# Performance work log

Hardware: AMD Instinct MI355X
Metric: run time of the kernel (lower is better)

## Reference

```python
import jax, jax.numpy as jnp
import numpy as np

DT = 0.1
WHEELBASE = 2.8
STATE_DIM = 12


def setup_inputs() -> dict:
    key = jax.random.key(0)
    k1, k2, k3 = jax.random.split(key, 3)
    b, l, h = 512, 64, 80
    x0 = jax.random.normal(k1, (b, STATE_DIM), dtype=jnp.float32)
    controls = jax.random.normal(k2, (b, l, h, 3), dtype=jnp.float32)
    deg = jax.random.uniform(k3, (b, 5), dtype=jnp.float32)
    return {"x0": x0, "controls": controls, "deg": deg}


def reference(x0, controls, deg):
    b, l, h, _ = controls.shape
    # degradation scales, broadcast over the l (candidate) dim: [b, 1]
    steer_scale = jnp.maximum(deg[:, 0:1], 0.05)
    brake_scale = jnp.maximum(deg[:, 1:2], 0.05)
    throttle_scale = jnp.maximum(deg[:, 2:3], 0.05)
    friction = jnp.maximum(deg[:, 4:5], 0.1)

    x_init = jnp.broadcast_to(x0[:, None, :], (b, l, x0.shape[-1]))  # [b,l,12]

    def step(x, u):  # x: [b,l,12], u: [b,l,3]
        delta = steer_scale * jnp.tanh(u[..., 0])
        fb = brake_scale * jax.nn.sigmoid(u[..., 1])
        fx = throttle_scale * jax.nn.sigmoid(u[..., 2])
        px, py, psi, vx, vy = (x[..., 0], x[..., 1], x[..., 2], x[..., 3], x[..., 4])
        speed = jnp.sqrt(vx * vx + vy * vy + 1e-06)
        acc = jnp.minimum(jnp.maximum(2.8 * fx - 6.5 * fb, -7.5 * friction), 3.0)
        speed2 = jnp.maximum(speed + acc * DT, 0.0)
        tan_d = jnp.tan(jnp.clip(delta, -0.75, 0.75))
        raw_yaw = speed2 / WHEELBASE * tan_d
        yaw_lim = jnp.maximum(friction * 9.81 / jnp.maximum(speed2, 2.0), 0.15)
        yaw_rate = jnp.clip(raw_yaw, -1.0, 1.0) * yaw_lim
        beta = jnp.clip(jnp.arctan(0.45 * tan_d), -0.65, 0.65)
        psi2 = psi + yaw_rate * DT
        vx2 = speed2 * jnp.cos(psi2 + beta)
        vy2 = speed2 * jnp.sin(psi2 + beta)
        px2 = px + vx2 * DT
        py2 = py + vy2 * DT
        ax = (vx2 - vx) / DT
        ay = (vy2 - vy) / DT
        x2 = jnp.stack([px2, py2, psi2, vx2, vy2, yaw_rate, ax, ay, beta, delta, fb, fx], -1)
        return x2, x2

    controls_t = jnp.moveaxis(controls, 2, 0)  # [h,b,l,3]
    _, traj = jax.lax.scan(step, x_init, controls_t)  # traj: [h,b,l,12]
    traj = jnp.concatenate([x_init[None], traj], axis=0)  # [h+1,b,l,12]
    return jnp.moveaxis(traj, 0, 2)  # [b,l,h+1,12]
```

## Files before the change

### kernel.cpp

```cpp
#include <hip/hip_runtime.h>
#include <math.h>


#define N_B 512
#define N_L 64
#define N_H 80
#define DT_F 0.1f
#define PITCH_F4 25
#define SPC 8
#define NCH 10
#define INV2PI 0.15915494309189535f

__device__ __forceinline__ float fast_rcp(float x) { return __builtin_amdgcn_rcpf(x); }

__device__ __forceinline__ float fast_tanh(float x) {
    const float e2 = __expf(2.0f * x);
    return (e2 - 1.0f) * fast_rcp(e2 + 1.0f);
}

__device__ __forceinline__ float fast_sigmoid(float x) {
    return fast_rcp(1.0f + __expf(-x));
}

__device__ __forceinline__ float fast_atan_small(float z) {
    const float z2 = z * z;
    float p = 1.0f / 9.0f;
    p = fmaf(p, z2, -1.0f / 7.0f);
    p = fmaf(p, z2, 1.0f / 5.0f);
    p = fmaf(p, z2, -1.0f / 3.0f);
    p = fmaf(p, z2, 1.0f);
    return z * p;
}

__device__ __forceinline__ float fast_tan_075(float x) {
    const float x2 = x * x;
    float p = 0.0035916f;
    p = fmaf(p, x2, 0.0088632f);
    p = fmaf(p, x2, 0.0218695f);
    p = fmaf(p, x2, 0.0539683f);
    p = fmaf(p, x2, 0.1333333f);
    p = fmaf(p, x2, 0.3333333f);
    return fmaf(p * x2, x, x);
}

struct Ctl { float delta, fb, fx, tan_d, beta, acc; };

__device__ __forceinline__ Ctl make_ctl(float u0, float u1, float u2,
                                        float steer_scale, float brake_scale,
                                        float throttle_scale, float neg_brake_lim) {
    Ctl t;
    t.delta = steer_scale * fast_tanh(u0);
    t.fb = brake_scale    * fast_sigmoid(u1);
    t.fx = throttle_scale * fast_sigmoid(u2);
    const float dc = fminf(fmaxf(t.delta, -0.75f), 0.75f);
    t.tan_d = fast_tan_075(dc);
    t.beta = fminf(fmaxf(fast_atan_small(0.45f * t.tan_d), -0.65f), 0.65f);
    t.acc = fminf(fmaxf(2.8f * t.fx - 6.5f * t.fb, neg_brake_lim), 3.0f);
    return t;
}

__global__ __launch_bounds__(512) void degraded_bicycle_rollout_kernel(
    const float* __restrict__ x0,
    const float* __restrict__ controls,
    const float* __restrict__ deg,
    float* __restrict__ out)
{
    __shared__ float4 lds4[2][2][N_L * PITCH_F4];

    const int lane = threadIdx.x & 63;
    const int wv   = threadIdx.x >> 6;

    const bool is_compute = (wv < 2);
    const int bb   = is_compute ? wv : ((wv - 2) & 1);
    const int slot = is_compute ? 0  : ((wv - 2) >> 1);

    const int b = blockIdx.x * 2 + bb;
    const size_t out_b = (size_t)b * 62208;

#define FLUSH_SLICE(BB, FBUF, FC, I0, I1)                                         \
    {                                                                             \
        const size_t obase = out_b + 12 + (size_t)(FC) * (SPC * 12);              \
        _Pragma("unroll")                                                         \
        for (int i = (I0); i < (I1); ++i) {                                       \
            const unsigned flat = i * 64 + lane;                                  \
            const unsigned l = flat / 24u;                                        \
            const unsigned q = flat - l * 24u;                                    \
            const float4 v = lds4[BB][FBUF][l * PITCH_F4 + q];                    \
            *reinterpret_cast<float4*>(out + obase + (size_t)l * 972 + q * 4) = v;\
        }                                                                         \
    }

    if (is_compute) {
        const float* dg = deg + b * 5;
        const float steer_scale    = fmaxf(dg[0], 0.05f);
        const float brake_scale    = fmaxf(dg[1], 0.05f);
        const float throttle_scale = fmaxf(dg[2], 0.05f);
        const float friction       = fmaxf(dg[4], 0.1f);

        const float4* x0v = reinterpret_cast<const float4*>(x0 + b * 12);
        const float4 xi0 = x0v[0];
        const float4 xi1 = x0v[1];

        float px  = xi0.x;
        float py  = xi0.y;
        float psi = xi0.z;
        float vxp = xi0.w;
        float vyp = xi1.x;
        float s = __builtin_amdgcn_sqrtf(fmaf(vxp, vxp, fmaf(vyp, vyp, 1e-6f)));

        const float neg_brake_lim = -7.5f * friction;
        const float yaw_num = friction * 9.81f;
        const float inv_wheelbase = 1.0f / 2.8f;

        const int tid = b * 64 + lane;
        const float4* uc = reinterpret_cast<const float4*>(controls + (size_t)tid * 240);

        float4 c0 = uc[0];
        float4 c1 = uc[1];
        float4 c2 = uc[2];

        for (int c = 0; c < NCH; ++c) {
            float4* lrow = &lds4[bb][c & 1][lane * PITCH_F4];

            #pragma unroll
            for (int gg = 0; gg < 2; ++gg) {
                const int g = c * 2 + gg;
                float4 n0 = c0, n1 = c1, n2 = c2;
                if (g < 19) {
                    n0 = uc[(g + 1) * 3 + 0];
                    n1 = uc[(g + 1) * 3 + 1];
                    n2 = uc[(g + 1) * 3 + 2];
                }

                const Ctl tA = make_ctl(c0.x, c0.y, c0.z, steer_scale, brake_scale, throttle_scale, neg_brake_lim);
                const Ctl tB = make_ctl(c0.w, c1.x, c1.y, steer_scale, brake_scale, throttle_scale, neg_brake_lim);
                const Ctl tC = make_ctl(c1.z, c1.w, c2.x, steer_scale, brake_scale, throttle_scale, neg_brake_lim);
                const Ctl tD = make_ctl(c2.y, c2.z, c2.w, steer_scale, brake_scale, throttle_scale, neg_brake_lim);

#define ROLL_STEP(T, RR)                                                          \
                {                                                                 \
                    const float s2 = fmaxf(fmaf((T).acc, DT_F, s), 0.0f);         \
                    const float raw_yaw = s2 * inv_wheelbase * (T).tan_d;         \
                    const float yaw_lim = fmaxf(yaw_num * fast_rcp(fmaxf(s2, 2.0f)), 0.15f); \
                    const float yaw_rate = fminf(fmaxf(raw_yaw, -1.0f), 1.0f) * yaw_lim; \
                    const float psi2 = fmaf(yaw_rate, DT_F, psi);                 \
                    const float ang = (psi2 + (T).beta) * INV2PI;                 \
                    const float sn = __builtin_amdgcn_sinf(ang);                  \
                    const float cs = __builtin_amdgcn_cosf(ang);                  \
                    const float vx2 = s2 * cs;                                    \
                    const float vy2 = s2 * sn;                                    \
                    const float px2 = fmaf(vx2, DT_F, px);                        \
                    const float py2 = fmaf(vy2, DT_F, py);                        \
                    const float ax = (vx2 - vxp) * 10.0f;                         \
                    const float ay = (vy2 - vyp) * 10.0f;                         \
                    lrow[(RR) * 3 + 0] = make_float4(px2, py2, psi2, vx2);        \
                    lrow[(RR) * 3 + 1] = make_float4(vy2, yaw_rate, ax, ay);      \
                    lrow[(RR) * 3 + 2] = make_float4((T).beta, (T).delta, (T).fb, (T).fx); \
                    s = __builtin_amdgcn_sqrtf(fmaf(s2, s2, 1e-6f));              \
                    px = px2; py = py2; psi = psi2; vxp = vx2; vyp = vy2;         \
                }

                ROLL_STEP(tA, gg * 4 + 0)
                ROLL_STEP(tB, gg * 4 + 1)
                ROLL_STEP(tC, gg * 4 + 2)
                ROLL_STEP(tD, gg * 4 + 3)
#undef ROLL_STEP

                c0 = n0; c1 = n1; c2 = n2;
            }
            __syncthreads();
        }
    } else {
        const int i0 = slot * 8;
        if (slot == 0) {
            const float4* x0v = reinterpret_cast<const float4*>(x0 + b * 12);
            const float4 xq0 = x0v[0];
            const float4 xq1 = x0v[1];
            const float4 xq2 = x0v[2];
            #pragma unroll
            for (int i = 0; i < 3; ++i) {
                const unsigned flat = i * 64 + lane;
                const unsigned l = flat / 3u;
                const unsigned q = flat - l * 3u;
                const float4 v = (q == 0) ? xq0 : (q == 1) ? xq1 : xq2;
                *reinterpret_cast<float4*>(out + out_b + (size_t)l * 972 + q * 4) = v;
            }
        }

        for (int c = 0; c < NCH; ++c) {
            __syncthreads();
            FLUSH_SLICE(bb, c & 1, c, i0, i0 + 8)
        }
    }
#undef FLUSH_SLICE
}

extern "C" void kernel_launch(void* const* d_in, const int* in_sizes, int n_in,
                              void* d_out, int out_size, void* d_ws, size_t ws_size,
                              hipStream_t stream) {
    (void)in_sizes; (void)n_in; (void)d_ws; (void)ws_size; (void)out_size;
    const float* x0       = (const float*)d_in[0];
    const float* controls = (const float*)d_in[1];
    const float* deg      = (const float*)d_in[2];
    float* out            = (float*)d_out;

    dim3 grid(N_B / 2), block(512);
    hipLaunchKernelGGL(degraded_bicycle_rollout_kernel, grid, block, 0, stream,
                       x0, controls, deg, out);
}
```

Measured before the change: 34.63 us.

## Offload control transforms to producer waves via LDS three-stage pipeline

```diff
diff --git a/kernel.cpp b/kernel.cpp
--- a/kernel.cpp
+++ b/kernel.cpp
@@ -43,59 +43,77 @@
     return fmaf(p * x2, x, x);
 }
 
-struct Ctl { float delta, fb, fx, tan_d, beta, acc; };
-
-__device__ __forceinline__ Ctl make_ctl(float u0, float u1, float u2,
-                                        float steer_scale, float brake_scale,
-                                        float throttle_scale, float neg_brake_lim) {
-    Ctl t;
-    t.delta = steer_scale * fast_tanh(u0);
-    t.fb = brake_scale    * fast_sigmoid(u1);
-    t.fx = throttle_scale * fast_sigmoid(u2);
-    const float dc = fminf(fmaxf(t.delta, -0.75f), 0.75f);
-    t.tan_d = fast_tan_075(dc);
-    t.beta = fminf(fmaxf(fast_atan_small(0.45f * t.tan_d), -0.65f), 0.65f);
-    t.acc = fminf(fmaxf(2.8f * t.fx - 6.5f * t.fb, neg_brake_lim), 3.0f);
-    return t;
-}
-
 __global__ __launch_bounds__(512) void degraded_bicycle_rollout_kernel(
     const float* __restrict__ x0,
     const float* __restrict__ controls,
     const float* __restrict__ deg,
     float* __restrict__ out)
 {
-    __shared__ float4 lds4[2][2][N_L * PITCH_F4];
+    __shared__ float4 outb[2][2][N_L * PITCH_F4];
+    __shared__ float  Abuf[2][2][512 * 3];
+    __shared__ float  Bbuf[2][2][512 * 3];
 
     const int lane = threadIdx.x & 63;
     const int wv   = threadIdx.x >> 6;
 
-    const bool is_compute = (wv < 2);
-    const int bb   = is_compute ? wv : ((wv - 2) & 1);
-    const int slot = is_compute ? 0  : ((wv - 2) >> 1);
-
-    const int b = blockIdx.x * 2 + bb;
+    const int role = (wv < 2) ? 0 : (wv < 6) ? 1 : 2;
+    const int bb   = (role == 0) ? wv : (role == 1) ? ((wv - 2) >> 1) : (wv - 6);
+    const int b    = blockIdx.x * 2 + bb;
     const size_t out_b = (size_t)b * 62208;
 
-#define FLUSH_SLICE(BB, FBUF, FC, I0, I1)                                         \
+#define FLUSH_CHUNK(BB, FBUF, FC)                                                 \
     {                                                                             \
         const size_t obase = out_b + 12 + (size_t)(FC) * (SPC * 12);              \
         _Pragma("unroll")                                                         \
-        for (int i = (I0); i < (I1); ++i) {                                       \
+        for (int i = 0; i < 24; ++i) {                                            \
             const unsigned flat = i * 64 + lane;                                  \
             const unsigned l = flat / 24u;                                        \
             const unsigned q = flat - l * 24u;                                    \
-            const float4 v = lds4[BB][FBUF][l * PITCH_F4 + q];                    \
+            const float4 v = outb[BB][FBUF][l * PITCH_F4 + q];                    \
             *reinterpret_cast<float4*>(out + obase + (size_t)l * 972 + q * 4) = v;\
         }                                                                         \
     }
 
-    if (is_compute) {
+#define CTL_CHUNK(PT, BB, PAR, CC)                                                \
+    {                                                                             \
+        const float* dgc = deg + (blockIdx.x * 2 + (BB)) * 5;                     \
+        const float steer_scale    = fmaxf(dgc[0], 0.05f);                        \
+        const float brake_scale    = fmaxf(dgc[1], 0.05f);                        \
+        const float throttle_scale = fmaxf(dgc[2], 0.05f);                        \
+        const float friction       = fmaxf(dgc[4], 0.1f);                         \
+        const float neg_brake_lim  = -7.5f * friction;                            \
+        _Pragma("unroll")                                                         \
+        for (int i = 0; i < 4; ++i) {                                             \
+            const int t = i * 128 + (PT);                             \
+            const int l = t >> 3;                                                 \
+            const int s = t & 7;                                                  \
+            const size_t gidx = ((size_t)((blockIdx.x * 2 + (BB)) * 64 + l) * 80  \
+                                 + (CC) * 8 + s) * 3;                             \
+            const float u0 = controls[gidx + 0];                                  \
+            const float u1 = controls[gidx + 1];                                  \
+            const float u2 = controls[gidx + 2];                                  \
+            const float delta = steer_scale * fast_tanh(u0);                      \
+            const float fb = brake_scale    * fast_sigmoid(u1);                   \
+            const float fx = throttle_scale * fast_sigmoid(u2);                   \
+            const float dc = fminf(fmaxf(delta, -0.75f), 0.75f);                  \
+            const float tan_d = fast_tan_075(dc);                                 \
+            const float beta = fminf(fmaxf(fast_atan_small(0.45f * tan_d), -0.65f), 0.65f); \
+            const float acc = fminf(fmaxf(2.8f * fx - 6.5f * fb, neg_brake_lim), 3.0f); \
+            const int e3 = (s * 64 + l) * 3;                                      \
+            Abuf[BB][PAR][e3 + 0] = tan_d;                                        \
+            Abuf[BB][PAR][e3 + 1] = beta;                                         \
+            Abuf[BB][PAR][e3 + 2] = acc;                                          \
+            Bbuf[BB][PAR][e3 + 0] = delta;                                        \
+            Bbuf[BB][PAR][e3 + 1] = fb;                                           \
+            Bbuf[BB][PAR][e3 + 2] = fx;                                           \
+        }                                                                         \
+    }
+
+    if (role == 0) {
         const float* dg = deg + b * 5;
-        const float steer_scale    = fmaxf(dg[0], 0.05f);
-        const float brake_scale    = fmaxf(dg[1], 0.05f);
-        const float throttle_scale = fmaxf(dg[2], 0.05f);
-        const float friction       = fmaxf(dg[4], 0.1f);
+        const float friction = fmaxf(dg[4], 0.1f);
+        const float yaw_num = friction * 9.81f;
+        const float inv_wheelbase = 1.0f / 2.8f;
 
         const float4* x0v = reinterpret_cast<const float4*>(x0 + b * 12);
         const float4 xi0 = x0v[0];
@@ -108,71 +126,58 @@
         float vyp = xi1.x;
         float s = __builtin_amdgcn_sqrtf(fmaf(vxp, vxp, fmaf(vyp, vyp, 1e-6f)));
 
-        const float neg_brake_lim = -7.5f * friction;
-        const float yaw_num = friction * 9.81f;
-        const float inv_wheelbase = 1.0f / 2.8f;
-
-        const int tid = b * 64 + lane;
-        const float4* uc = reinterpret_cast<const float4*>(controls + (size_t)tid * 240);
-
-        float4 c0 = uc[0];
-        float4 c1 = uc[1];
-        float4 c2 = uc[2];
+        __syncthreads();
 
         for (int c = 0; c < NCH; ++c) {
-            float4* lrow = &lds4[bb][c & 1][lane * PITCH_F4];
+            const int par = c & 1;
+            float4* lrow = &outb[bb][par][lane * PITCH_F4];
+            const float* Ab = &Abuf[bb][par][lane * 3];
+            const float* Bb = &Bbuf[bb][par][lane * 3];
 
             #pragma unroll
-            for (int gg = 0; gg < 2; ++gg) {
-                const int g = c * 2 + gg;
-                float4 n0 = c0, n1 = c1, n2 = c2;
-                if (g < 19) {
-                    n0 = uc[(g + 1) * 3 + 0];
-                    n1 = uc[(g + 1) * 3 + 1];
-                    n2 = uc[(g + 1) * 3 + 2];
-                }
-
-                const Ctl tA = make_ctl(c0.x, c0.y, c0.z, steer_scale, brake_scale, throttle_scale, neg_brake_lim);
-                const Ctl tB = make_ctl(c0.w, c1.x, c1.y, steer_scale, brake_scale, throttle_scale, neg_brake_lim);
-                const Ctl tC = make_ctl(c1.z, c1.w, c2.x, steer_scale, brake_scale, throttle_scale, neg_brake_lim);
-                const Ctl tD = make_ctl(c2.y, c2.z, c2.w, steer_scale, brake_scale, throttle_scale, neg_brake_lim);
-
-#define ROLL_STEP(T, RR)                                                          \
-                {                                                                 \
-                    const float s2 = fmaxf(fmaf((T).acc, DT_F, s), 0.0f);         \
-                    const float raw_yaw = s2 * inv_wheelbase * (T).tan_d;         \
-                    const float yaw_lim = fmaxf(yaw_num * fast_rcp(fmaxf(s2, 2.0f)), 0.15f); \
-                    const float yaw_rate = fminf(fmaxf(raw_yaw, -1.0f), 1.0f) * yaw_lim; \
-                    const float psi2 = fmaf(yaw_rate, DT_F, psi);                 \
-                    const float ang = (psi2 + (T).beta) * INV2PI;                 \
-                    const float sn = __builtin_amdgcn_sinf(ang);                  \
-                    const float cs = __builtin_amdgcn_cosf(ang);                  \
-                    const float vx2 = s2 * cs;                                    \
-                    const float vy2 = s2 * sn;                                    \
-                    const float px2 = fmaf(vx2, DT_F, px);                        \
-                    const float py2 = fmaf(vy2, DT_F, py);                        \
-                    const float ax = (vx2 - vxp) * 10.0f;                         \
-                    const float ay = (vy2 - vyp) * 10.0f;                         \
-                    lrow[(RR) * 3 + 0] = make_float4(px2, py2, psi2, vx2);        \
-                    lrow[(RR) * 3 + 1] = make_float4(vy2, yaw_rate, ax, ay);      \
-                    lrow[(RR) * 3 + 2] = make_float4((T).beta, (T).delta, (T).fb, (T).fx); \
-                    s = __builtin_amdgcn_sqrtf(fmaf(s2, s2, 1e-6f));              \
-                    px = px2; py = py2; psi = psi2; vxp = vx2; vyp = vy2;         \
-                }
-
-                ROLL_STEP(tA, gg * 4 + 0)
-                ROLL_STEP(tB, gg * 4 + 1)
-                ROLL_STEP(tC, gg * 4 + 2)
-                ROLL_STEP(tD, gg * 4 + 3)
-#undef ROLL_STEP
-
-                c0 = n0; c1 = n1; c2 = n2;
+            for (int st = 0; st < SPC; ++st) {
+                const float tan_d = Ab[st * 192 + 0];
+                const float beta  = Ab[st * 192 + 1];
+                const float acc   = Ab[st * 192 + 2];
+                const float delta = Bb[st * 192 + 0];
+                const float fb    = Bb[st * 192 + 1];
+                const float fx    = Bb[st * 192 + 2];
+
+                const float s2 = fmaxf(fmaf(acc, DT_F, s), 0.0f);
+                const float raw_yaw = s2 * inv_wheelbase * tan_d;
+                const float yaw_lim = fmaxf(yaw_num * fast_rcp(fmaxf(s2, 2.0f)), 0.15f);
+                const float yaw_rate = fminf(fmaxf(raw_yaw, -1.0f), 1.0f) * yaw_lim;
+                const float psi2 = fmaf(yaw_rate, DT_F, psi);
+                const float ang = (psi2 + beta) * INV2PI;
+                const float sn = __builtin_amdgcn_sinf(ang);
+                const float cs = __builtin_amdgcn_cosf(ang);
+                const float vx2 = s2 * cs;
+                const float vy2 = s2 * sn;
+                const float px2 = fmaf(vx2, DT_F, px);
+                const float py2 = fmaf(vy2, DT_F, py);
+                const float ax = (vx2 - vxp) * 10.0f;
+                const float ay = (vy2 - vyp) * 10.0f;
+
+                lrow[st * 3 + 0] = make_float4(px2, py2, psi2, vx2);
+                lrow[st * 3 + 1] = make_float4(vy2, yaw_rate, ax, ay);
+                lrow[st * 3 + 2] = make_float4(beta, delta, fb, fx);
+
+                s = __builtin_amdgcn_sqrtf(fmaf(s2, s2, 1e-6f));
+                px = px2; py = py2; psi = psi2; vxp = vx2; vyp = vy2;
             }
             __syncthreads();
         }
+    } else if (role == 1) {
+        const int pt = ((wv - 2) & 1) * 64 + lane;
+        CTL_CHUNK(pt, bb, 0, 0)
+        __syncthreads();
+
+        for (int c = 0; c < NCH; ++c) {
+            if (c + 1 < NCH) CTL_CHUNK(pt, bb, (c + 1) & 1, c + 1)
+            __syncthreads();
+        }
     } else {
-        const int i0 = slot * 8;
-        if (slot == 0) {
+        {
             const float4* x0v = reinterpret_cast<const float4*>(x0 + b * 12);
             const float4 xq0 = x0v[0];
             const float4 xq1 = x0v[1];
@@ -186,13 +191,16 @@
                 *reinterpret_cast<float4*>(out + out_b + (size_t)l * 972 + q * 4) = v;
             }
         }
+        __syncthreads();
 
         for (int c = 0; c < NCH; ++c) {
+            if (c > 0) FLUSH_CHUNK(bb, (c - 1) & 1, c - 1)
             __syncthreads();
-            FLUSH_SLICE(bb, c & 1, c, i0, i0 + 8)
-        }
+        }
+        FLUSH_CHUNK(bb, (NCH - 1) & 1, NCH - 1)
     }
-#undef FLUSH_SLICE
+#undef FLUSH_CHUNK
+#undef CTL_CHUNK
 }
 
 extern "C" void kernel_launch(void* const* d_in, const int* in_sizes, int n_in,
```

Measured after the change: 35.32 us. No clear change (+2.0%).

## Interleave two batch rollouts in one compute wave, three store waves

Applied to the files above, without the earlier changes.

```diff
diff --git a/kernel.cpp b/kernel.cpp
--- a/kernel.cpp
+++ b/kernel.cpp
@@ -59,140 +59,153 @@
     return t;
 }
 
-__global__ __launch_bounds__(512) void degraded_bicycle_rollout_kernel(
+__global__ __launch_bounds__(256) void degraded_bicycle_rollout_kernel(
     const float* __restrict__ x0,
     const float* __restrict__ controls,
     const float* __restrict__ deg,
     float* __restrict__ out)
 {
-    __shared__ float4 lds4[2][2][N_L * PITCH_F4];
+    __shared__ float4 outb[2][2][N_L * PITCH_F4];
 
     const int lane = threadIdx.x & 63;
     const int wv   = threadIdx.x >> 6;
-
-    const bool is_compute = (wv < 2);
-    const int bb   = is_compute ? wv : ((wv - 2) & 1);
-    const int slot = is_compute ? 0  : ((wv - 2) >> 1);
-
-    const int b = blockIdx.x * 2 + bb;
-    const size_t out_b = (size_t)b * 62208;
-
-#define FLUSH_SLICE(BB, FBUF, FC, I0, I1)                                         \
+    const int b0 = blockIdx.x * 2;
+
+#define FLUSH_SLICES(FBUF, FC, S0, S1)                                            \
     {                                                                             \
-        const size_t obase = out_b + 12 + (size_t)(FC) * (SPC * 12);              \
         _Pragma("unroll")                                                         \
-        for (int i = (I0); i < (I1); ++i) {                                       \
+        for (int sl = (S0); sl < (S1); ++sl) {                                    \
+            const int fbb = sl / 24;                                              \
+            const int i = sl - fbb * 24;                                          \
+            const size_t obase = (size_t)(b0 + fbb) * 62208 + 12                  \
+                                 + (size_t)(FC) * (SPC * 12);                     \
             const unsigned flat = i * 64 + lane;                                  \
             const unsigned l = flat / 24u;                                        \
             const unsigned q = flat - l * 24u;                                    \
-            const float4 v = lds4[BB][FBUF][l * PITCH_F4 + q];                    \
+            const float4 v = outb[fbb][FBUF][l * PITCH_F4 + q];                   \
             *reinterpret_cast<float4*>(out + obase + (size_t)l * 972 + q * 4) = v;\
         }                                                                         \
     }
 
-    if (is_compute) {
-        const float* dg = deg + b * 5;
-        const float steer_scale    = fmaxf(dg[0], 0.05f);
-        const float brake_scale    = fmaxf(dg[1], 0.05f);
-        const float throttle_scale = fmaxf(dg[2], 0.05f);
-        const float friction       = fmaxf(dg[4], 0.1f);
-
-        const float4* x0v = reinterpret_cast<const float4*>(x0 + b * 12);
-        const float4 xi0 = x0v[0];
-        const float4 xi1 = x0v[1];
-
-        float px  = xi0.x;
-        float py  = xi0.y;
-        float psi = xi0.z;
-        float vxp = xi0.w;
-        float vyp = xi1.x;
-        float s = __builtin_amdgcn_sqrtf(fmaf(vxp, vxp, fmaf(vyp, vyp, 1e-6f)));
-
-        const float neg_brake_lim = -7.5f * friction;
-        const float yaw_num = friction * 9.81f;
-        const float inv_wheelbase = 1.0f / 2.8f;
-
-        const int tid = b * 64 + lane;
-        const float4* uc = reinterpret_cast<const float4*>(controls + (size_t)tid * 240);
-
-        float4 c0 = uc[0];
-        float4 c1 = uc[1];
-        float4 c2 = uc[2];
+    if (wv == 0) {
+        const float* dgA = deg + (b0 + 0) * 5;
+        const float* dgB = deg + (b0 + 1) * 5;
+        const float ssA = fmaxf(dgA[0], 0.05f), ssB = fmaxf(dgB[0], 0.05f);
+        const float bsA = fmaxf(dgA[1], 0.05f), bsB = fmaxf(dgB[1], 0.05f);
+        const float tsA = fmaxf(dgA[2], 0.05f), tsB = fmaxf(dgB[2], 0.05f);
+        const float frA = fmaxf(dgA[4], 0.1f),  frB = fmaxf(dgB[4], 0.1f);
+        const float nbA = -7.5f * frA, nbB = -7.5f * frB;
+        const float ynA = frA * 9.81f, ynB = frB * 9.81f;
+        const float inv_wb = 1.0f / 2.8f;
+
+        const float4* xA = reinterpret_cast<const float4*>(x0 + (b0 + 0) * 12);
+        const float4* xB = reinterpret_cast<const float4*>(x0 + (b0 + 1) * 12);
+        const float4 a0 = xA[0], a1 = xA[1];
+        const float4 b0v = xB[0], b1v = xB[1];
+
+        float pxA = a0.x, pyA = a0.y, psiA = a0.z, vxA = a0.w, vyA = a1.x;
+        float pxB = b0v.x, pyB = b0v.y, psiB = b0v.z, vxB = b0v.w, vyB = b1v.x;
+        float sA = __builtin_amdgcn_sqrtf(fmaf(vxA, vxA, fmaf(vyA, vyA, 1e-6f)));
+        float sB = __builtin_amdgcn_sqrtf(fmaf(vxB, vxB, fmaf(vyB, vyB, 1e-6f)));
+
+        const float4* ucA = reinterpret_cast<const float4*>(controls + ((size_t)(b0 + 0) * 64 + lane) * 240);
+        const float4* ucB = reinterpret_cast<const float4*>(controls + ((size_t)(b0 + 1) * 64 + lane) * 240);
+
+        float4 cA0 = ucA[0], cA1 = ucA[1], cA2 = ucA[2];
+        float4 cB0 = ucB[0], cB1 = ucB[1], cB2 = ucB[2];
 
         for (int c = 0; c < NCH; ++c) {
-            float4* lrow = &lds4[bb][c & 1][lane * PITCH_F4];
+            const int par = c & 1;
+            float4* lrowA = &outb[0][par][lane * PITCH_F4];
+            float4* lrowB = &outb[1][par][lane * PITCH_F4];
 
             #pragma unroll
             for (int gg = 0; gg < 2; ++gg) {
                 const int g = c * 2 + gg;
-                float4 n0 = c0, n1 = c1, n2 = c2;
+                float4 nA0 = cA0, nA1 = cA1, nA2 = cA2;
+                float4 nB0 = cB0, nB1 = cB1, nB2 = cB2;
                 if (g < 19) {
-                    n0 = uc[(g + 1) * 3 + 0];
-                    n1 = uc[(g + 1) * 3 + 1];
-                    n2 = uc[(g + 1) * 3 + 2];
+                    nA0 = ucA[(g + 1) * 3 + 0];
+                    nA1 = ucA[(g + 1) * 3 + 1];
+                    nA2 = ucA[(g + 1) * 3 + 2];
+                    nB0 = ucB[(g + 1) * 3 + 0];
+                    nB1 = ucB[(g + 1) * 3 + 1];
+                    nB2 = ucB[(g + 1) * 3 + 2];
                 }
 
-                const Ctl tA = make_ctl(c0.x, c0.y, c0.z, steer_scale, brake_scale, throttle_scale, neg_brake_lim);
-                const Ctl tB = make_ctl(c0.w, c1.x, c1.y, steer_scale, brake_scale, throttle_scale, neg_brake_lim);
-                const Ctl tC = make_ctl(c1.z, c1.w, c2.x, steer_scale, brake_scale, throttle_scale, neg_brake_lim);
-                const Ctl tD = make_ctl(c2.y, c2.z, c2.w, steer_scale, brake_scale, throttle_scale, neg_brake_lim);
-
-#define ROLL_STEP(T, RR)                                                          \
+                const Ctl tA0 = make_ctl(cA0.x, cA0.y, cA0.z, ssA, bsA, tsA, nbA);
+                const Ctl tB0 = make_ctl(cB0.x, cB0.y, cB0.z, ssB, bsB, tsB, nbB);
+                const Ctl tA1 = make_ctl(cA0.w, cA1.x, cA1.y, ssA, bsA, tsA, nbA);
+                const Ctl tB1 = make_ctl(cB0.w, cB1.x, cB1.y, ssB, bsB, tsB, nbB);
+                const Ctl tA2 = make_ctl(cA1.z, cA1.w, cA2.x, ssA, bsA, tsA, nbA);
+                const Ctl tB2 = make_ctl(cB1.z, cB1.w, cB2.x, ssB, bsB, tsB, nbB);
+                const Ctl tA3 = make_ctl(cA2.y, cA2.z, cA2.w, ssA, bsA, tsA, nbA);
+                const Ctl tB3 = make_ctl(cB2.y, cB2.z, cB2.w, ssB, bsB, tsB, nbB);
+
+#define STEP1(T, S, PX, PY, PSI, VX, VY, YN, LROW, RR)                            \
                 {                                                                 \
-                    const float s2 = fmaxf(fmaf((T).acc, DT_F, s), 0.0f);         \
-                    const float raw_yaw = s2 * inv_wheelbase * (T).tan_d;         \
-                    const float yaw_lim = fmaxf(yaw_num * fast_rcp(fmaxf(s2, 2.0f)), 0.15f); \
+                    const float s2 = fmaxf(fmaf((T).acc, DT_F, S), 0.0f);         \
+                    const float raw_yaw = s2 * inv_wb * (T).tan_d;                \
+                    const float yaw_lim = fmaxf((YN) * fast_rcp(fmaxf(s2, 2.0f)), 0.15f); \
                     const float yaw_rate = fminf(fmaxf(raw_yaw, -1.0f), 1.0f) * yaw_lim; \
-                    const float psi2 = fmaf(yaw_rate, DT_F, psi);                 \
+                    const float psi2 = fmaf(yaw_rate, DT_F, PSI);                 \
                     const float ang = (psi2 + (T).beta) * INV2PI;                 \
                     const float sn = __builtin_amdgcn_sinf(ang);                  \
                     const float cs = __builtin_amdgcn_cosf(ang);                  \
                     const float vx2 = s2 * cs;                                    \
                     const float vy2 = s2 * sn;                                    \
-                    const float px2 = fmaf(vx2, DT_F, px);                        \
-                    const float py2 = fmaf(vy2, DT_F, py);                        \
-                    const float ax = (vx2 - vxp) * 10.0f;                         \
-                    const float ay = (vy2 - vyp) * 10.0f;                         \
-                    lrow[(RR) * 3 + 0] = make_float4(px2, py2, psi2, vx2);        \
-                    lrow[(RR) * 3 + 1] = make_float4(vy2, yaw_rate, ax, ay);      \
-                    lrow[(RR) * 3 + 2] = make_float4((T).beta, (T).delta, (T).fb, (T).fx); \
-                    s = __builtin_amdgcn_sqrtf(fmaf(s2, s2, 1e-6f));              \
-                    px = px2; py = py2; psi = psi2; vxp = vx2; vyp = vy2;         \
+                    const float px2 = fmaf(vx2, DT_F, PX);                        \
+                    const float py2 = fmaf(vy2, DT_F, PY);                        \
+                    const float ax = (vx2 - (VX)) * 10.0f;                        \
+                    const float ay = (vy2 - (VY)) * 10.0f;                        \
+                    (LROW)[(RR) * 3 + 0] = make_float4(px2, py2, psi2, vx2);      \
+                    (LROW)[(RR) * 3 + 1] = make_float4(vy2, yaw_rate, ax, ay);    \
+                    (LROW)[(RR) * 3 + 2] = make_float4((T).beta, (T).delta, (T).fb, (T).fx); \
+                    S = __builtin_amdgcn_sqrtf(fmaf(s2, s2, 1e-6f));              \
+                    PX = px2; PY = py2; PSI = psi2; VX = vx2; VY = vy2;           \
                 }
 
-                ROLL_STEP(tA, gg * 4 + 0)
-                ROLL_STEP(tB, gg * 4 + 1)
-                ROLL_STEP(tC, gg * 4 + 2)
-                ROLL_STEP(tD, gg * 4 + 3)
-#undef ROLL_STEP
-
-                c0 = n0; c1 = n1; c2 = n2;
+                STEP1(tA0, sA, pxA, pyA, psiA, vxA, vyA, ynA, lrowA, gg * 4 + 0)
+                STEP1(tB0, sB, pxB, pyB, psiB, vxB, vyB, ynB, lrowB, gg * 4 + 0)
+                STEP1(tA1, sA, pxA, pyA, psiA, vxA, vyA, ynA, lrowA, gg * 4 + 1)
+                STEP1(tB1, sB, pxB, pyB, psiB, vxB, vyB, ynB, lrowB, gg * 4 + 1)
+                STEP1(tA2, sA, pxA, pyA, psiA, vxA, vyA, ynA, lrowA, gg * 4 + 2)
+                STEP1(tB2, sB, pxB, pyB, psiB, vxB, vyB, ynB, lrowB, gg * 4 + 2)
+                STEP1(tA3, sA, pxA, pyA, psiA, vxA, vyA, ynA, lrowA, gg * 4 + 3)
+                STEP1(tB3, sB, pxB, pyB, psiB, vxB, vyB, ynB, lrowB, gg * 4 + 3)
+#undef STEP1
+
+                cA0 = nA0; cA1 = nA1; cA2 = nA2;
+                cB0 = nB0; cB1 = nB1; cB2 = nB2;
             }
             __syncthreads();
         }
     } else {
-        const int i0 = slot * 8;
-        if (slot == 0) {
-            const float4* x0v = reinterpret_cast<const float4*>(x0 + b * 12);
-            const float4 xq0 = x0v[0];
-            const float4 xq1 = x0v[1];
-            const float4 xq2 = x0v[2];
-            #pragma unroll
-            for (int i = 0; i < 3; ++i) {
-                const unsigned flat = i * 64 + lane;
-                const unsigned l = flat / 3u;
-                const unsigned q = flat - l * 3u;
-                const float4 v = (q == 0) ? xq0 : (q == 1) ? xq1 : xq2;
-                *reinterpret_cast<float4*>(out + out_b + (size_t)l * 972 + q * 4) = v;
+        const int s0 = (wv - 1) * 16;
+        {
+            if (wv <= 2) {
+                const int bh = b0 + (wv - 1);
+                const float4* x0v = reinterpret_cast<const float4*>(x0 + bh * 12);
+                const float4 xq0 = x0v[0];
+                const float4 xq1 = x0v[1];
+                const float4 xq2 = x0v[2];
+                #pragma unroll
+                for (int i = 0; i < 3; ++i) {
+                    const unsigned flat = i * 64 + lane;
+                    const unsigned l = flat / 3u;
+                    const unsigned q = flat - l * 3u;
+                    const float4 v = (q == 0) ? xq0 : (q == 1) ? xq1 : xq2;
+                    *reinterpret_cast<float4*>(out + (size_t)bh * 62208 + (size_t)l * 972 + q * 4) = v;
+                }
             }
         }
 
         for (int c = 0; c < NCH; ++c) {
             __syncthreads();
-            FLUSH_SLICE(bb, c & 1, c, i0, i0 + 8)
+            FLUSH_SLICES(c & 1, c, s0, s0 + 16)
         }
     }
-#undef FLUSH_SLICE
+#undef FLUSH_SLICES
 }
 
 extern "C" void kernel_launch(void* const* d_in, const int* in_sizes, int n_in,
@@ -204,7 +217,7 @@
     const float* deg      = (const float*)d_in[2];
     float* out            = (float*)d_out;
 
-    dim3 grid(N_B / 2), block(512);
+    dim3 grid(N_B / 2), block(256);
     hipLaunchKernelGGL(degraded_bicycle_rollout_kernel, grid, block, 0, stream,
                        x0, controls, deg, out);
 }
```

New measurement: 39.33 us. +13.6%, slower.

## Replace per-step sin/cos with angle-addition recurrence and share one reciprocal

Applied to the files above, without the earlier changes.

```diff
diff --git a/kernel.cpp b/kernel.cpp
--- a/kernel.cpp
+++ b/kernel.cpp
@@ -12,15 +12,6 @@
 #define INV2PI 0.15915494309189535f
 
 __device__ __forceinline__ float fast_rcp(float x) { return __builtin_amdgcn_rcpf(x); }
-
-__device__ __forceinline__ float fast_tanh(float x) {
-    const float e2 = __expf(2.0f * x);
-    return (e2 - 1.0f) * fast_rcp(e2 + 1.0f);
-}
-
-__device__ __forceinline__ float fast_sigmoid(float x) {
-    return fast_rcp(1.0f + __expf(-x));
-}
 
 __device__ __forceinline__ float fast_atan_small(float z) {
     const float z2 = z * z;
@@ -43,18 +34,37 @@
     return fmaf(p * x2, x, x);
 }
 
-struct Ctl { float delta, fb, fx, tan_d, beta, acc; };
+struct Ctl { float delta, fb, fx, tan_d, beta, acc, sb, cb; };
 
 __device__ __forceinline__ Ctl make_ctl(float u0, float u1, float u2,
                                         float steer_scale, float brake_scale,
                                         float throttle_scale, float neg_brake_lim) {
     Ctl t;
-    t.delta = steer_scale * fast_tanh(u0);
-    t.fb = brake_scale    * fast_sigmoid(u1);
-    t.fx = throttle_scale * fast_sigmoid(u2);
+    const float e2 = __expf(2.0f * u0);
+    const float eb = __expf(-u1);
+    const float ec = __expf(-u2);
+    const float a  = e2 + 1.0f;
+    const float bd = 1.0f + eb;
+    const float cd = 1.0f + ec;
+    const float bc = bd * cd;
+    const float invP = fast_rcp(a * bc);
+    t.delta = steer_scale * ((e2 - 1.0f) * (invP * bc));
+    t.fb = brake_scale    * (invP * (a * cd));
+    t.fx = throttle_scale * (invP * (a * bd));
+
     const float dc = fminf(fmaxf(t.delta, -0.75f), 0.75f);
     t.tan_d = fast_tan_075(dc);
-    t.beta = fminf(fmaxf(fast_atan_small(0.45f * t.tan_d), -0.65f), 0.65f);
+    const float z = 0.45f * t.tan_d;
+    t.beta = fast_atan_small(z);
+
+    const float b2 = t.beta * t.beta;
+    float ps = fmaf(b2, 1.0f / 120.0f, -1.0f / 6.0f);
+    ps = fmaf(b2, ps, 1.0f);
+    t.sb = t.beta * ps;
+    float pcc = fmaf(b2, -1.0f / 720.0f, 1.0f / 24.0f);
+    float pc  = fmaf(b2, pcc, -0.5f);
+    t.cb = fmaf(b2, pc, 1.0f);
+
     t.acc = fminf(fmaxf(2.8f * t.fx - 6.5f * t.fb, neg_brake_lim), 3.0f);
     return t;
 }
@@ -107,6 +117,8 @@
         float vxp = xi0.w;
         float vyp = xi1.x;
         float s = __builtin_amdgcn_sqrtf(fmaf(vxp, vxp, fmaf(vyp, vyp, 1e-6f)));
+        float sp = __builtin_amdgcn_sinf(psi * INV2PI);
+        float cp = __builtin_amdgcn_cosf(psi * INV2PI);
 
         const float neg_brake_lim = -7.5f * friction;
         const float yaw_num = friction * 9.81f;
@@ -144,9 +156,19 @@
                     const float yaw_lim = fmaxf(yaw_num * fast_rcp(fmaxf(s2, 2.0f)), 0.15f); \
                     const float yaw_rate = fminf(fmaxf(raw_yaw, -1.0f), 1.0f) * yaw_lim; \
                     const float psi2 = fmaf(yaw_rate, DT_F, psi);                 \
-                    const float ang = (psi2 + (T).beta) * INV2PI;                 \
-                    const float sn = __builtin_amdgcn_sinf(ang);                  \
-                    const float cs = __builtin_amdgcn_cosf(ang);                  \
+                      \
+                    const float d  = yaw_rate * DT_F;            \
+                    const float d2 = d * d;                                       \
+                    float qs = fmaf(d2, 1.0f / 120.0f, -1.0f / 6.0f);             \
+                    const float sd = d * fmaf(d2, qs, 1.0f);                      \
+                    float qc = fmaf(d2, -1.0f / 720.0f, 1.0f / 24.0f);            \
+                    qc = fmaf(d2, qc, -0.5f);                                     \
+                    const float cdd = fmaf(d2, qc, 1.0f);                         \
+                    const float spn = fmaf(sp, cdd, cp * sd);                     \
+                    const float cpn = fmaf(cp, cdd, -(sp * sd));                  \
+                                        \
+                    const float sn = fmaf(spn, (T).cb, cpn * (T).sb);             \
+                    const float cs = fmaf(cpn, (T).cb, -(spn * (T).sb));          \
                     const float vx2 = s2 * cs;                                    \
                     const float vy2 = s2 * sn;                                    \
                     const float px2 = fmaf(vx2, DT_F, px);                        \
@@ -156,8 +178,9 @@
                     lrow[(RR) * 3 + 0] = make_float4(px2, py2, psi2, vx2);        \
                     lrow[(RR) * 3 + 1] = make_float4(vy2, yaw_rate, ax, ay);      \
                     lrow[(RR) * 3 + 2] = make_float4((T).beta, (T).delta, (T).fb, (T).fx); \
-                    s = __builtin_amdgcn_sqrtf(fmaf(s2, s2, 1e-6f));              \
+                    s = fmaxf(s2, 1e-3f);               \
                     px = px2; py = py2; psi = psi2; vxp = vx2; vyp = vy2;         \
+                    sp = spn; cp = cpn;                                           \
                 }
 
                 ROLL_STEP(tA, gg * 4 + 0)
```

Measured after the change: 35.57 us. 2.7% more time.
